# Kernel tuning notes

Measured on AMD Instinct MI355X. Metric: run time of the kernel, lower is better.

Reference implementation:

```python
import jax, jax.numpy as jnp
import numpy as np

N_ENT = 1_000_000
N_REL = 200
D = 128
B = 16384


def setup_inputs() -> dict:
    key = jax.random.key(0)
    k1, k2, k3, k4, k5, k6, k7 = jax.random.split(key, 7)
    heads = jax.random.randint(k1, (B,), 0, N_ENT)
    tails = jax.random.randint(k2, (B,), 0, N_ENT)
    negative_heads = jax.random.randint(k3, (B,), 0, N_ENT)
    negative_tails = jax.random.randint(k4, (B,), 0, N_ENT)
    relations = jax.random.randint(k5, (B,), 0, N_REL)
    # entity embeddings: xavier_uniform then L2-normalized rows (as in __init__)
    ent = jax.random.normal(k6, (N_ENT, D), dtype=jnp.float32)
    ent = ent / jnp.linalg.norm(ent, axis=1, keepdims=True)
    rel_mats = jax.random.normal(k7, (N_REL, D, D), dtype=jnp.float32) * 0.05
    return {
        "heads": heads,
        "tails": tails,
        "negative_heads": negative_heads,
        "negative_tails": negative_tails,
        "relations": relations,
        "ent_emb": ent,
        "rel_mats": rel_mats,
    }


def _bilinear(h, r, t):
    # h: [B, D], r: [B, D, D], t: [B, D] -> [B] score h^T R t
    return jnp.einsum("bd,bde,be->b", h, r, t)


def reference(heads, tails, negative_heads, negative_tails, relations, ent_emb, rel_mats):
    h = ent_emb[heads]               # [B, D]
    t = ent_emb[tails]               # [B, D]
    nh = ent_emb[negative_heads]     # [B, D]
    nt = ent_emb[negative_tails]     # [B, D]
    r = rel_mats[relations]          # [B, D, D]
    return _bilinear(h, r, t), _bilinear(nh, r, nt)
```

## Files before the change

### kernel.cpp

```cpp
#include <hip/hip_runtime.h>


#define NB    16384
#define D     128
#define NREL  200
#define SPLIT 4
#define NT    4
#define TV    (2*NT)

__global__ __launch_bounds__(1024) void rescal_bucket(
    const int* __restrict__ rel, int* __restrict__ order, int* __restrict__ start)
{
    __shared__ int cnt[NREL];
    __shared__ int cur[NREL];
    const int tid = threadIdx.x;
    for (int i = tid; i < NREL; i += 1024) cnt[i] = 0;
    __syncthreads();
    for (int i = tid; i < NB; i += 1024) atomicAdd(&cnt[rel[i]], 1);
    __syncthreads();
    if (tid <= NREL) {
        int s = 0;
        for (int k = 0; k < NREL; ++k) { int c = cnt[k]; s += (k < tid) ? c : 0; }
        start[tid] = s;
        if (tid < NREL) cur[tid] = s;
    }
    __syncthreads();
    for (int i = tid; i < NB; i += 1024) {
        int p = atomicAdd(&cur[rel[i]], 1);
        order[p] = i;
    }
}

__global__ __launch_bounds__(256, 2) void rescal_score(
    const int* __restrict__ heads, const int* __restrict__ tails,
    const int* __restrict__ nheads, const int* __restrict__ ntails,
    const float* __restrict__ ent, const float* __restrict__ relm,
    const int* __restrict__ order, const int* __restrict__ start,
    float* __restrict__ out)
{
    __shared__ __align__(16) float Rlds[D * D];
    __shared__ __align__(16) float tlds[4][TV][D];

    const int tid  = threadIdx.x;
    const int wave = tid >> 6;
    const int lane = tid & 63;
    const int r = blockIdx.x % NREL;
    const int j = blockIdx.x / NREL;

    {
        const float4* Rg = (const float4*)(relm + (size_t)r * (D * D));
        char* Rb = (char*)Rlds;
        #pragma unroll
        for (int k = 0; k < (D * D / 4) / 256; ++k) {
            int idx = tid + k * 256;
            unsigned lin = (unsigned)idx * 16u;
            unsigned swz = lin ^ (((lin >> 9) & 7u) << 4);
            *(float4*)(Rb + swz) = Rg[idx];
        }
    }

    const int bs = start[r];
    const int n  = start[r + 1] - bs;
    __syncthreads();
    if (n == 0) return;
    const int per   = (n + SPLIT - 1) / SPLIT;
    const int mybeg = j * per;
    const int mycnt = min(n - mybeg, per);
    if (mycnt <= 0) return;

    const unsigned xsw   = (unsigned)(lane & 7) << 4;
    const unsigned baseA = (unsigned)lane * (D * 4);
    const unsigned baseB = (unsigned)(lane + 64) * (D * 4);
    const char* Rb = (const char*)Rlds;

    for (int s0 = wave * NT; s0 < mycnt; s0 += 4 * NT) {
        int trip[NT];
        #pragma unroll
        for (int q = 0; q < NT; ++q) {
            int s = s0 + q; if (s >= mycnt) s = mycnt - 1;
            trip[q] = order[bs + mybeg + s];
        }

        {
            int v = lane >> 3;
            int q = v >> 1;
            const int* idxa = (v & 1) ? ntails : tails;
            const float4* src = (const float4*)(ent + (size_t)idxa[trip[q]] * D);
            float4* dst = (float4*)(&tlds[wave][v][0]);
            int f = lane & 7;
            #pragma unroll
            for (int k = 0; k < 4; ++k) dst[f + 8 * k] = src[f + 8 * k];
        }

        float h0[TV], h1[TV];
        #pragma unroll
        for (int v = 0; v < TV; ++v) {
            int q = v >> 1;
            const int* idxa = (v & 1) ? nheads : heads;
            const float* hrow = ent + (size_t)idxa[trip[q]] * D;
            h0[v] = hrow[lane];
            h1[v] = hrow[lane + 64];
        }

        float acc0[TV], acc1[TV];
        #pragma unroll
        for (int v = 0; v < TV; ++v) { acc0[v] = 0.f; acc1[v] = 0.f; }

        #pragma unroll 4
        for (int e0 = 0; e0 < D; e0 += 4) {
            float4 ra = *(const float4*)(Rb + ((baseA + e0 * 4) ^ xsw));
            float4 rb = *(const float4*)(Rb + ((baseB + e0 * 4) ^ xsw));
            #pragma unroll
            for (int v = 0; v < TV; ++v) {
                float4 tv = *(const float4*)(&tlds[wave][v][e0]);
                acc0[v] += ra.x * tv.x + ra.y * tv.y + ra.z * tv.z + ra.w * tv.w;
                acc1[v] += rb.x * tv.x + rb.y * tv.y + rb.z * tv.z + rb.w * tv.w;
            }
        }

        #pragma unroll
        for (int v = 0; v < TV; ++v) {
            float p = h0[v] * acc0[v] + h1[v] * acc1[v];
            #pragma unroll
            for (int m = 32; m >= 1; m >>= 1) p += __shfl_xor(p, m, 64);
            if (lane == 0) {
                int s = s0 + (v >> 1);
                if (s < mycnt) {
                    float* o = (v & 1) ? (out + NB) : out;
                    o[trip[v >> 1]] = p;
                }
            }
        }
    }
}

extern "C" void kernel_launch(void* const* d_in, const int* in_sizes, int n_in,
                              void* d_out, int out_size, void* d_ws, size_t ws_size,
                              hipStream_t stream)
{
    const int*   heads  = (const int*)d_in[0];
    const int*   tails  = (const int*)d_in[1];
    const int*   nheads = (const int*)d_in[2];
    const int*   ntails = (const int*)d_in[3];
    const int*   rels   = (const int*)d_in[4];
    const float* ent    = (const float*)d_in[5];
    const float* relm   = (const float*)d_in[6];
    float* out = (float*)d_out;

    int* order = (int*)d_ws;
    int* start = order + NB;

    rescal_bucket<<<1, 1024, 0, stream>>>(rels, order, start);
    rescal_score<<<NREL * SPLIT, 256, 0, stream>>>(heads, tails, nheads, ntails,
                                                   ent, relm, order, start, out);
}
```

Measured before the change: 632.6 us.

## Replace bucket-sort kernel with in-block ballot scan and async LDS loads

Drops the single-block bucketing kernel. Each score block now scans its quarter of the relation array with wave ballots and builds a per-wave list of matching indices in LDS, capped at 64 per wave. The relation matrix and tail rows are copied straight into LDS with global_load_lds. Tail rows are staged in two halves to shrink the LDS buffer. This removes a serial launch and the global order/start indirection, but every block now rescans 4096 relation ids, and any wave with more than 64 matches silently loses entries.

Measured after the change: 640.7 us. Within noise of the previous version (+1.3%).

```diff
diff --git a/kernel.cpp b/kernel.cpp
--- a/kernel.cpp
+++ b/kernel.cpp
@@ -5,41 +5,27 @@
 #define D     128
 #define NREL  200
 #define SPLIT 4
+#define RANGE (NB/SPLIT)
 #define NT    4
 #define TV    (2*NT)
 
-__global__ __launch_bounds__(1024) void rescal_bucket(
-    const int* __restrict__ rel, int* __restrict__ order, int* __restrict__ start)
-{
-    __shared__ int cnt[NREL];
-    __shared__ int cur[NREL];
-    const int tid = threadIdx.x;
-    for (int i = tid; i < NREL; i += 1024) cnt[i] = 0;
-    __syncthreads();
-    for (int i = tid; i < NB; i += 1024) atomicAdd(&cnt[rel[i]], 1);
-    __syncthreads();
-    if (tid <= NREL) {
-        int s = 0;
-        for (int k = 0; k < NREL; ++k) { int c = cnt[k]; s += (k < tid) ? c : 0; }
-        start[tid] = s;
-        if (tid < NREL) cur[tid] = s;
-    }
-    __syncthreads();
-    for (int i = tid; i < NB; i += 1024) {
-        int p = atomicAdd(&cur[rel[i]], 1);
-        order[p] = i;
-    }
+typedef const __attribute__((address_space(1))) char gchar;
+typedef __attribute__((address_space(3))) char       lchar;
+
+__device__ __forceinline__ void gload_lds16(const void* g, void* l) {
+    __builtin_amdgcn_global_load_lds((gchar*)g, (lchar*)l, 16, 0, 0);
 }
 
 __global__ __launch_bounds__(256, 2) void rescal_score(
     const int* __restrict__ heads, const int* __restrict__ tails,
     const int* __restrict__ nheads, const int* __restrict__ ntails,
-    const float* __restrict__ ent, const float* __restrict__ relm,
-    const int* __restrict__ order, const int* __restrict__ start,
-    float* __restrict__ out)
+    const int* __restrict__ rel, const float* __restrict__ ent,
+    const float* __restrict__ relm, float* __restrict__ out)
 {
     __shared__ __align__(16) float Rlds[D * D];
-    __shared__ __align__(16) float tlds[4][TV][D];
+    __shared__ __align__(16) float tlds[4][TV][64];
+    __shared__ int list[4][64];
+    __shared__ int wcnt[4];
 
     const int tid  = threadIdx.x;
     const int wave = tid >> 6;
@@ -47,57 +33,69 @@
     const int r = blockIdx.x % NREL;
     const int j = blockIdx.x / NREL;
 
-    {
-        const float4* Rg = (const float4*)(relm + (size_t)r * (D * D));
-        char* Rb = (char*)Rlds;
-        #pragma unroll
-        for (int k = 0; k < (D * D / 4) / 256; ++k) {
-            int idx = tid + k * 256;
-            unsigned lin = (unsigned)idx * 16u;
-            unsigned swz = lin ^ (((lin >> 9) & 7u) << 4);
-            *(float4*)(Rb + swz) = Rg[idx];
-        }
+    const char* Rg = (const char*)(relm + (size_t)r * (D * D));
+    char* Rb = (char*)Rlds;
+    #pragma unroll
+    for (int k = 0; k < 16; ++k) {
+        unsigned dst = (unsigned)k * 4096u + (unsigned)wave * 1024u;
+        unsigned lin = dst + (unsigned)lane * 16u;
+        unsigned src = lin ^ (((lin >> 9) & 7u) << 4);
+        gload_lds16(Rg + src, Rb + dst);
     }
 
-    const int bs = start[r];
-    const int n  = start[r + 1] - bs;
+    {
+        const int base = j * RANGE + wave * (RANGE / 4);
+        int tot = 0;
+        #pragma unroll
+        for (int rd = 0; rd < (RANGE / 4) / 64; ++rd) {
+            int i = base + rd * 64 + lane;
+            bool m = (rel[i] == r);
+            unsigned long long mask = __ballot(m);
+            if (m) {
+                int pos = tot + __popcll(mask & ((1ull << lane) - 1ull));
+                if (pos < 64) list[wave][pos] = i;
+            }
+            tot += __popcll(mask);
+        }
+        if (lane == 0) wcnt[wave] = (tot < 64) ? tot : 64;
+    }
     __syncthreads();
-    if (n == 0) return;
-    const int per   = (n + SPLIT - 1) / SPLIT;
-    const int mybeg = j * per;
-    const int mycnt = min(n - mybeg, per);
-    if (mycnt <= 0) return;
 
-    const unsigned xsw   = (unsigned)(lane & 7) << 4;
-    const unsigned baseA = (unsigned)lane * (D * 4);
-    const unsigned baseB = (unsigned)(lane + 64) * (D * 4);
-    const char* Rb = (const char*)Rlds;
+    const int c0 = wcnt[0], c1 = wcnt[1], c2 = wcnt[2], c3 = wcnt[3];
+    const int cnt = c0 + c1 + c2 + c3;
 
-    for (int s0 = wave * NT; s0 < mycnt; s0 += 4 * NT) {
+    const unsigned xsw  = ((unsigned)(lane & 7)) << 4;
+    const unsigned rowA = (unsigned)lane * 512u;
+    const unsigned rowB = (unsigned)(lane + 64) * 512u;
+
+    const int vA = lane >> 4;
+    const int fo = (lane & 15) * 4;
+
+    for (int s0 = wave * NT; s0 < cnt; s0 += 4 * NT) {
         int trip[NT];
         #pragma unroll
         for (int q = 0; q < NT; ++q) {
-            int s = s0 + q; if (s >= mycnt) s = mycnt - 1;
-            trip[q] = order[bs + mybeg + s];
+            int s = s0 + q; if (s >= cnt) s = cnt - 1;
+            int a = s, seg = 0;
+            if (a >= c0) { a -= c0; seg = 1;
+              if (a >= c1) { a -= c1; seg = 2;
+                if (a >= c2) { a -= c2; seg = 3; } } }
+            trip[q] = list[seg][a];
         }
 
-        {
-            int v = lane >> 3;
-            int q = v >> 1;
-            const int* idxa = (v & 1) ? ntails : tails;
-            const float4* src = (const float4*)(ent + (size_t)idxa[trip[q]] * D);
-            float4* dst = (float4*)(&tlds[wave][v][0]);
-            int f = lane & 7;
-            #pragma unroll
-            for (int k = 0; k < 4; ++k) dst[f + 8 * k] = src[f + 8 * k];
-        }
+        const int* selT = (vA & 1) ? ntails : tails;
+        const float* srcA = ent + (size_t)selT[trip[vA >> 1]]       * D + fo;
+        const float* srcB = ent + (size_t)selT[trip[2 + (vA >> 1)]] * D + fo;
+
+        asm volatile("s_waitcnt lgkmcnt(0)" ::: "memory");
+        gload_lds16(srcA,      &tlds[wave][0][0]);
+        gload_lds16(srcB,      &tlds[wave][4][0]);
 
         float h0[TV], h1[TV];
         #pragma unroll
         for (int v = 0; v < TV; ++v) {
-            int q = v >> 1;
-            const int* idxa = (v & 1) ? nheads : heads;
-            const float* hrow = ent + (size_t)idxa[trip[q]] * D;
+            const int* sel = (v & 1) ? nheads : heads;
+            const float* hrow = ent + (size_t)sel[trip[v >> 1]] * D;
             h0[v] = hrow[lane];
             h1[v] = hrow[lane + 64];
         }
@@ -106,15 +104,34 @@
         #pragma unroll
         for (int v = 0; v < TV; ++v) { acc0[v] = 0.f; acc1[v] = 0.f; }
 
+        asm volatile("s_waitcnt vmcnt(0)" ::: "memory");
+
         #pragma unroll 4
-        for (int e0 = 0; e0 < D; e0 += 4) {
-            float4 ra = *(const float4*)(Rb + ((baseA + e0 * 4) ^ xsw));
-            float4 rb = *(const float4*)(Rb + ((baseB + e0 * 4) ^ xsw));
+        for (int e0 = 0; e0 < 64; e0 += 4) {
+            float4 ra = *(const float4*)(Rb + ((rowA + e0 * 4) ^ xsw));
+            float4 rb = *(const float4*)(Rb + ((rowB + e0 * 4) ^ xsw));
             #pragma unroll
             for (int v = 0; v < TV; ++v) {
-                float4 tv = *(const float4*)(&tlds[wave][v][e0]);
-                acc0[v] += ra.x * tv.x + ra.y * tv.y + ra.z * tv.z + ra.w * tv.w;
-                acc1[v] += rb.x * tv.x + rb.y * tv.y + rb.z * tv.z + rb.w * tv.w;
+                float4 t4 = *(const float4*)(&tlds[wave][v][e0]);
+                acc0[v] += ra.x * t4.x + ra.y * t4.y + ra.z * t4.z + ra.w * t4.w;
+                acc1[v] += rb.x * t4.x + rb.y * t4.y + rb.z * t4.z + rb.w * t4.w;
+            }
+        }
+
+        asm volatile("s_waitcnt lgkmcnt(0)" ::: "memory");
+        gload_lds16(srcA + 64, &tlds[wave][0][0]);
+        gload_lds16(srcB + 64, &tlds[wave][4][0]);
+        asm volatile("s_waitcnt vmcnt(0)" ::: "memory");
+
+        #pragma unroll 4
+        for (int e0 = 0; e0 < 64; e0 += 4) {
+            float4 ra = *(const float4*)(Rb + ((rowA + 256 + e0 * 4) ^ xsw));
+            float4 rb = *(const float4*)(Rb + ((rowB + 256 + e0 * 4) ^ xsw));
+            #pragma unroll
+            for (int v = 0; v < TV; ++v) {
+                float4 t4 = *(const float4*)(&tlds[wave][v][e0]);
+                acc0[v] += ra.x * t4.x + ra.y * t4.y + ra.z * t4.z + ra.w * t4.w;
+                acc1[v] += rb.x * t4.x + rb.y * t4.y + rb.z * t4.z + rb.w * t4.w;
             }
         }
 
@@ -125,7 +142,7 @@
             for (int m = 32; m >= 1; m >>= 1) p += __shfl_xor(p, m, 64);
             if (lane == 0) {
                 int s = s0 + (v >> 1);
-                if (s < mycnt) {
+                if (s < cnt) {
                     float* o = (v & 1) ? (out + NB) : out;
                     o[trip[v >> 1]] = p;
                 }
@@ -147,10 +164,6 @@
     const float* relm   = (const float*)d_in[6];
     float* out = (float*)d_out;
 
-    int* order = (int*)d_ws;
-    int* start = order + NB;
-
-    rescal_bucket<<<1, 1024, 0, stream>>>(rels, order, start);
     rescal_score<<<NREL * SPLIT, 256, 0, stream>>>(heads, tails, nheads, ntails,
-                                                   ent, relm, order, start, out);
+                                                   rels, ent, relm, out);
 }
```
